# Kernel tuning notes

Measured on AMD Instinct MI355X. Metric: run time of the kernel, lower is better.

## Reference

```python
import jax, jax.numpy as jnp
import numpy as np

B, C, T, N = 8, 64, 24, 512
H = 2
D = C // H  # 32
NEG = -1e9
LN_EPS = 1e-5


def setup_inputs() -> dict:
    key = jax.random.key(0)
    ks = jax.random.split(key, 8)
    s = 1.0 / np.sqrt(C)
    return {
        "x": jax.random.normal(ks[0], (B, C, T, N), jnp.float32),
        "gso": jax.random.randint(ks[1], (N, N), 0, 2, jnp.int32),
        "Wq": jax.random.normal(ks[2], (C, C), jnp.float32) * s,
        "Wk": jax.random.normal(ks[3], (C, C), jnp.float32) * s,
        "Wv": jax.random.normal(ks[4], (C, C), jnp.float32) * s,
        "a_src": jax.random.normal(ks[5], (H, D), jnp.float32) * s,
        "a_dst": jax.random.normal(ks[6], (H, D), jnp.float32) * s,
        "gamma": jnp.ones((C,), jnp.float32),
        "beta": jnp.zeros((C,), jnp.float32),
    }


def reference(x, gso, Wq, Wk, Wv, a_src, a_dst, gamma, beta):
    # x: (B, C, T, N) -> (M, N, C) with M = B*T
    xr = jnp.transpose(x, (0, 2, 3, 1)).reshape(B * T, N, C)
    # torch Linear: y = x @ W.T ; split heads -> (M, N, H, D)
    Q = jnp.einsum('mnc,dc->mnd', xr, Wq).reshape(B * T, N, H, D)
    K = jnp.einsum('mnc,dc->mnd', xr, Wk).reshape(B * T, N, H, D)
    V = jnp.einsum('mnc,dc->mnd', xr, Wv).reshape(B * T, N, H, D)
    # additive GAT scores: s_ij = leaky_relu(<q_i, a_src> + <k_j, a_dst>)
    s_src = jnp.einsum('mnhd,hd->mhn', Q, a_src)  # (M, H, N)
    s_dst = jnp.einsum('mnhd,hd->mhn', K, a_dst)  # (M, H, N)
    scores = s_src[:, :, :, None] + s_dst[:, :, None, :]  # (M, H, N, N)
    scores = jax.nn.leaky_relu(scores, negative_slope=0.2)
    mask = jnp.where(gso == 0, jnp.float32(NEG), jnp.float32(0.0))  # (N, N)
    scores = scores + mask[None, None, :, :]
    attn = jax.nn.softmax(scores, axis=-1)  # dropout is identity in eval
    out = jnp.einsum('mhij,mjhd->mihd', attn, V).reshape(B * T, N, C)
    # LayerNorm over channels
    mu = jnp.mean(out, axis=-1, keepdims=True)
    var = jnp.var(out, axis=-1, keepdims=True)
    out = (out - mu) * jax.lax.rsqrt(var + LN_EPS) * gamma + beta
    # (M, N, C) -> (B, C, T, N)
    return jnp.transpose(out.reshape(B, T, N, C), (0, 3, 1, 2))
```

## Files before the change

### kernel.cpp

```cpp
#include <hip/hip_runtime.h>
#include <hip/hip_bf16.h>


#define NB 8
#define NC 64
#define NT 24
#define NN 512
#define LOG2E 1.44269504088896f

typedef float f32x4 __attribute__((ext_vector_type(4)));
typedef short bf16x8 __attribute__((ext_vector_type(8)));
typedef int   i32x4 __attribute__((ext_vector_type(4)));
typedef unsigned int u32;
typedef u32 u32x2 __attribute__((ext_vector_type(2)));

#ifndef __has_builtin
#define __has_builtin(x) 0
#endif

__device__ __forceinline__ float fast_exp2(float x) {
#if __has_builtin(__builtin_amdgcn_exp2f)
    return __builtin_amdgcn_exp2f(x);
#else
    return exp2f(x);
#endif
}

__device__ __forceinline__ u32 pk_bf16(float lo, float hi) {
    __hip_bfloat162 h2 = __float22bfloat162_rn(float2{lo, hi});
    u32 r; __builtin_memcpy(&r, &h2, 4); return r;
}
__device__ __forceinline__ unsigned short f2bfh(float f) {
    __hip_bfloat16 h = __float2bfloat16(f);
    unsigned short r; __builtin_memcpy(&r, &h, 2); return r;
}
__device__ __forceinline__ float bf2f(unsigned short s) {
    union { unsigned int u; float f; } v;
    v.u = ((unsigned int)s) << 16;
    return v.f;
}

#define VT2_IDX(k2,h,qq,dt,dl,e) \
    ((((((k2)*2+(h))*4+(qq))*2+(dt))*16+(dl))*8+(e))

#define XRB64(n,c) (((n)<<6) + (((((c)>>3) ^ ((n)&7))<<3) | ((c)&7)))

__global__ __launch_bounds__(512, 6)
void gat_one(const float* __restrict__ x, const int* __restrict__ gso,
             const float* __restrict__ Wq, const float* __restrict__ Wk,
             const float* __restrict__ Wv, const float* __restrict__ a_src,
             const float* __restrict__ a_dst, const float* __restrict__ gamma,
             const float* __restrict__ beta, float* __restrict__ out)
{
    __shared__ unsigned short sm_x[4096];
    __shared__ unsigned short sm_v[16384];
    __shared__ unsigned short sm_wvb[4096];
    __shared__ float sm_sdst[2][256];
    __shared__ float sm_ssrc[2][128];
    __shared__ float sm_wqa[2][NC];
    __shared__ float sm_wka[2][NC];

    const int bid  = blockIdx.x;
    const int m    = (bid >> 5) * 8 + (bid & 7);
    const int ch   = (bid >> 3) & 3;
    const int b    = m / NT;
    const int tt   = m % NT;
    const int tid  = threadIdx.x;
    const int lane = tid & 63;
    const int wid  = tid >> 6;
    const int fr   = lane & 15;
    const int fq   = lane >> 4;

    if (tid < 128) {
        const int h = tid >> 6, c = tid & 63;
        float aq = 0.f, ak = 0.f;
        #pragma unroll
        for (int d = 0; d < 32; ++d) {
            aq += Wq[(h*32 + d)*NC + c] * a_src[h*32 + d];
            ak += Wk[(h*32 + d)*NC + c] * a_dst[h*32 + d];
        }
        sm_wqa[h][c] = aq * LOG2E;
        sm_wka[h][c] = ak * LOG2E;
    }
    for (int idx = tid; idx < 4096; idx += 512) {
        const int e   = idx & 7;
        const int dl  = (idx >> 3) & 15;
        const int dt4 = (idx >> 7) & 3;
        const int qq  = (idx >> 9) & 3;
        const int ks  = idx >> 11;
        sm_wvb[idx] = f2bfh(Wv[(dt4*16 + dl)*NC + ks*32 + qq*8 + e]);
    }

    bf16x8 bones;
    {
        union { i32x4 i; bf16x8 h; } cv;
        const int w = (fr == 0) ? 0x3F803F80 : 0;
        cv.i[0] = w; cv.i[1] = w; cv.i[2] = w; cv.i[3] = w;
        bones = cv.h;
    }

    const int own_half = ch >> 1;
    const int ig = ch*128 + wid*16 + fr;
    float src0 = 0.f, src1 = 0.f;

    f32x4 acc[4] = {};
    f32x4 accs0 = {}, accs1 = {};

    #pragma unroll
    for (int pass = 0; pass < 2; ++pass) {
        const int hf = pass ? (1 - own_half) : own_half;

        for (int cidx = 0; cidx < 4; ++cidx) {
            const int nh0 = cidx * 64;
            const int ng0 = hf*256 + nh0;

            __syncthreads();

            {
                const int cb = wid * 8;
                float v[8];
                #pragma unroll
                for (int e = 0; e < 8; ++e)
                    v[e] = x[((size_t)(b*NC + cb + e)*NT + tt)*NN + ng0 + lane];
                i32x4 w;
                #pragma unroll
                for (int j = 0; j < 4; ++j)
                    w[j] = (int)pk_bf16(v[2*j], v[2*j+1]);
                *reinterpret_cast<i32x4*>(&sm_x[XRB64(lane, cb)]) = w;
            }
            __syncthreads();

            {
                const int nloc = tid >> 3;
                const int cp   = tid & 7;
                float sk0=0.f, sk1=0.f, sq0=0.f, sq1=0.f;
                #pragma unroll
                for (int i = 0; i < 8; ++i) {
                    const int c = cp*8 + i;
                    const float xv = bf2f(sm_x[XRB64(nloc, c)]);
                    sk0 += xv * sm_wka[0][c];
                    sk1 += xv * sm_wka[1][c];
                    sq0 += xv * sm_wqa[0][c];
                    sq1 += xv * sm_wqa[1][c];
                }
                sk0 += __shfl_xor(sk0,1); sk0 += __shfl_xor(sk0,2); sk0 += __shfl_xor(sk0,4);
                sk1 += __shfl_xor(sk1,1); sk1 += __shfl_xor(sk1,2); sk1 += __shfl_xor(sk1,4);
                sq0 += __shfl_xor(sq0,1); sq0 += __shfl_xor(sq0,2); sq0 += __shfl_xor(sq0,4);
                sq1 += __shfl_xor(sq1,1); sq1 += __shfl_xor(sq1,2); sq1 += __shfl_xor(sq1,4);
                if (cp == 0) {
                    sm_sdst[0][nh0 + nloc] = sk0;
                    sm_sdst[1][nh0 + nloc] = sk1;
                    if (pass == 0 && (cidx >> 1) == (ch & 1)) {
                        sm_ssrc[0][(cidx & 1)*64 + nloc] = sq0;
                        sm_ssrc[1][(cidx & 1)*64 + nloc] = sq1;
                    }
                }
            }

            {
                const int t = wid >> 1;
                const int h = wid & 1;
                f32x4 vacc[2] = {};
                #pragma unroll
                for (int ks = 0; ks < 2; ++ks) {
                    const bf16x8 af = *reinterpret_cast<const bf16x8*>(
                        &sm_x[XRB64(t*16 + fr, ks*32 + fq*8)]);
                    #pragma unroll
                    for (int dt = 0; dt < 2; ++dt) {
                        const int dt4 = h*2 + dt;
                        const bf16x8 bfv = *reinterpret_cast<const bf16x8*>(
                            &sm_wvb[(((ks*4 + fq)*4 + dt4)*16 + fr)*8]);
                        vacc[dt] = __builtin_amdgcn_mfma_f32_16x16x32_bf16(
                            af, bfv, vacc[dt], 0, 0, 0);
                    }
                }
                const int nh = nh0 + t*16 + 4*fq;
                #pragma unroll
                for (int dt = 0; dt < 2; ++dt) {
                    u32x2 dd;
                    dd[0] = pk_bf16(vacc[dt][0], vacc[dt][1]);
                    dd[1] = pk_bf16(vacc[dt][2], vacc[dt][3]);
                    *reinterpret_cast<u32x2*>(
                        &sm_v[VT2_IDX(nh>>5, h, (nh>>3)&3, dt, fr, nh&7)]) = dd;
                }
            }
        }
        __syncthreads();

        if (pass == 0) {
            src0 = sm_ssrc[0][wid*16 + fr];
            src1 = sm_ssrc[1][wid*16 + fr];
        }

        const int* gbase = &gso[(size_t)ig*NN + hf*256 + fq*8];
        for (int k2 = 0; k2 < 8; ++k2) {
            const int j0l = k2*32 + fq*8;
            const i32x4 g0 = *reinterpret_cast<const i32x4*>(gbase + k2*32);
            const i32x4 g1 = *reinterpret_cast<const i32x4*>(gbase + k2*32 + 4);
            const f32x4 da0 = *reinterpret_cast<const f32x4*>(&sm_sdst[0][j0l]);
            const f32x4 db0 = *reinterpret_cast<const f32x4*>(&sm_sdst[0][j0l+4]);
            const f32x4 da1 = *reinterpret_cast<const f32x4*>(&sm_sdst[1][j0l]);
            const f32x4 db1 = *reinterpret_cast<const f32x4*>(&sm_sdst[1][j0l+4]);

            u32 u0[8], u1[8];
            #pragma unroll
            for (int e = 0; e < 4; ++e) {
                float s0 = src0 + da0[e]; s0 = fmaxf(s0, 0.2f*s0);
                float s1 = src1 + da1[e]; s1 = fmaxf(s1, 0.2f*s1);
                const bool gb = (g0[e] != 0);
                u0[e] = gb ? __float_as_uint(fast_exp2(s0)) : 0u;
                u1[e] = gb ? __float_as_uint(fast_exp2(s1)) : 0u;
            }
            #pragma unroll
            for (int e = 0; e < 4; ++e) {
                float s0 = src0 + db0[e]; s0 = fmaxf(s0, 0.2f*s0);
                float s1 = src1 + db1[e]; s1 = fmaxf(s1, 0.2f*s1);
                const bool gb = (g1[e] != 0);
                u0[4+e] = gb ? __float_as_uint(fast_exp2(s0)) : 0u;
                u1[4+e] = gb ? __float_as_uint(fast_exp2(s1)) : 0u;
            }
            union { i32x4 i; bf16x8 h; } c0, c1;
            c0.i[0] = __builtin_amdgcn_perm(u0[1], u0[0], 0x07060302u);
            c0.i[1] = __builtin_amdgcn_perm(u0[3], u0[2], 0x07060302u);
            c0.i[2] = __builtin_amdgcn_perm(u0[5], u0[4], 0x07060302u);
            c0.i[3] = __builtin_amdgcn_perm(u0[7], u0[6], 0x07060302u);
            c1.i[0] = __builtin_amdgcn_perm(u1[1], u1[0], 0x07060302u);
            c1.i[1] = __builtin_amdgcn_perm(u1[3], u1[2], 0x07060302u);
            c1.i[2] = __builtin_amdgcn_perm(u1[5], u1[4], 0x07060302u);
            c1.i[3] = __builtin_amdgcn_perm(u1[7], u1[6], 0x07060302u);
            const bf16x8 af0 = c0.h, af1 = c1.h;

            accs0 = __builtin_amdgcn_mfma_f32_16x16x32_bf16(af0, bones, accs0, 0,0,0);
            {
                const bf16x8 b0 = *reinterpret_cast<const bf16x8*>(
                    &sm_v[VT2_IDX(k2,0,fq,0,fr,0)]);
                const bf16x8 b1 = *reinterpret_cast<const bf16x8*>(
                    &sm_v[VT2_IDX(k2,0,fq,1,fr,0)]);
                acc[0] = __builtin_amdgcn_mfma_f32_16x16x32_bf16(af0, b0, acc[0], 0,0,0);
                acc[1] = __builtin_amdgcn_mfma_f32_16x16x32_bf16(af0, b1, acc[1], 0,0,0);
            }
            accs1 = __builtin_amdgcn_mfma_f32_16x16x32_bf16(af1, bones, accs1, 0,0,0);
            {
                const bf16x8 b0 = *reinterpret_cast<const bf16x8*>(
                    &sm_v[VT2_IDX(k2,1,fq,0,fr,0)]);
                const bf16x8 b1 = *reinterpret_cast<const bf16x8*>(
                    &sm_v[VT2_IDX(k2,1,fq,1,fr,0)]);
                acc[2] = __builtin_amdgcn_mfma_f32_16x16x32_bf16(af1, b0, acc[2], 0,0,0);
                acc[3] = __builtin_amdgcn_mfma_f32_16x16x32_bf16(af1, b1, acc[3], 0,0,0);
            }
        }
    }

    float gmv[4], btv[4];
    #pragma unroll
    for (int dt4 = 0; dt4 < 4; ++dt4) {
        gmv[dt4] = gamma[dt4*16 + fr];
        btv[dt4] = beta [dt4*16 + fr];
    }
    #pragma unroll
    for (int rg = 0; rg < 4; ++rg) {
        const int rowloc = 4*fq + rg;
        const float rs0 = __shfl(accs0[rg], lane & 48);
        const float rs1 = __shfl(accs1[rg], lane & 48);
        const float inv0 = 1.f / rs0, inv1 = 1.f / rs1;
        float vv[4];
        vv[0] = acc[0][rg] * inv0;
        vv[1] = acc[1][rg] * inv0;
        vv[2] = acc[2][rg] * inv1;
        vv[3] = acc[3][rg] * inv1;
        float sum = vv[0]+vv[1]+vv[2]+vv[3];
        float ssq = vv[0]*vv[0]+vv[1]*vv[1]+vv[2]*vv[2]+vv[3]*vv[3];
        sum += __shfl_xor(sum,1); sum += __shfl_xor(sum,2);
        sum += __shfl_xor(sum,4); sum += __shfl_xor(sum,8);
        ssq += __shfl_xor(ssq,1); ssq += __shfl_xor(ssq,2);
        ssq += __shfl_xor(ssq,4); ssq += __shfl_xor(ssq,8);
        const float mu   = sum * (1.f/64.f);
        const float var  = ssq * (1.f/64.f) - mu*mu;
        const float rstd = rsqrtf(var + 1e-5f);
        const int irow = ch*128 + wid*16 + rowloc;
        #pragma unroll
        for (int dt4 = 0; dt4 < 4; ++dt4) {
            const float o = (vv[dt4] - mu) * rstd * gmv[dt4] + btv[dt4];
            out[((size_t)(b*NC + dt4*16 + fr)*NT + tt)*NN + irow] = o;
        }
    }
}

extern "C" void kernel_launch(void* const* d_in, const int* in_sizes, int n_in,
                              void* d_out, int out_size, void* d_ws, size_t ws_size,
                              hipStream_t stream) {
    (void)in_sizes; (void)n_in; (void)out_size; (void)d_ws; (void)ws_size;
    const float* x     = (const float*)d_in[0];
    const int*   gso   = (const int*)  d_in[1];
    const float* Wq    = (const float*)d_in[2];
    const float* Wk    = (const float*)d_in[3];
    const float* Wv    = (const float*)d_in[4];
    const float* a_src = (const float*)d_in[5];
    const float* a_dst = (const float*)d_in[6];
    const float* gamma = (const float*)d_in[7];
    const float* beta  = (const float*)d_in[8];
    float* out = (float*)d_out;

    gat_one<<<768, 512, 0, stream>>>(x, gso, Wq, Wk, Wv, a_src, a_dst,
                                     gamma, beta, out);
}
```

Measured before the change: 55.47 us.

## Factor leaky-relu exp into per-node exponentials and pipeline x loads over quarter chunks

The per-edge exp2 of leaky_relu(src+dst) is rewritten as max(E_i*F_j, E'_i*F'_j), where per-node exponentials for slope 1 and slope 0.2 are precomputed once per node. This removes transcendental work from the inner N×N loop. The loop now runs over four quarters of 128 nodes instead of two halves, which halves sm_v and allows 8 waves per SIMD in the launch bounds. The next chunk of x is register-prefetched so global loads overlap the compute. The risks are overflow or underflow in the factored exponentials, since there is no max subtraction, and more register pressure under the tighter occupancy bound.

```diff
diff --git a/kernel.cpp b/kernel.cpp
--- a/kernel.cpp
+++ b/kernel.cpp
@@ -45,7 +45,7 @@
 
 #define XRB64(n,c) (((n)<<6) + (((((c)>>3) ^ ((n)&7))<<3) | ((c)&7)))
 
-__global__ __launch_bounds__(512, 6)
+__global__ __launch_bounds__(512, 8)
 void gat_one(const float* __restrict__ x, const int* __restrict__ gso,
              const float* __restrict__ Wq, const float* __restrict__ Wk,
              const float* __restrict__ Wv, const float* __restrict__ a_src,
@@ -53,10 +53,10 @@
              const float* __restrict__ beta, float* __restrict__ out)
 {
     __shared__ unsigned short sm_x[4096];
-    __shared__ unsigned short sm_v[16384];
+    __shared__ unsigned short sm_v[8192];
     __shared__ unsigned short sm_wvb[4096];
-    __shared__ float sm_sdst[2][256];
-    __shared__ float sm_ssrc[2][128];
+    __shared__ float sm_sdst[2][2][128];
+    __shared__ float sm_ssrc[2][2][128];
     __shared__ float sm_wqa[2][NC];
     __shared__ float sm_wka[2][NC];
 
@@ -99,34 +99,43 @@
         bones = cv.h;
     }
 
-    const int own_half = ch >> 1;
     const int ig = ch*128 + wid*16 + fr;
-    float src0 = 0.f, src1 = 0.f;
-
+    const size_t xrow = ((size_t)(b*NC + wid*8)*NT + tt)*NN;
+
+    float vx[8];
+    {
+        const int ng0 = ch*128;
+        #pragma unroll
+        for (int e = 0; e < 8; ++e)
+            vx[e] = x[xrow + (size_t)e*NT*NN + ng0 + lane];
+    }
+
+    float Ei0 = 0.f, Ei0p = 0.f, Ei1 = 0.f, Ei1p = 0.f;
     f32x4 acc[4] = {};
     f32x4 accs0 = {}, accs1 = {};
 
-    #pragma unroll
-    for (int pass = 0; pass < 2; ++pass) {
-        const int hf = pass ? (1 - own_half) : own_half;
-
-        for (int cidx = 0; cidx < 4; ++cidx) {
-            const int nh0 = cidx * 64;
-            const int ng0 = hf*256 + nh0;
-
+    for (int t = 0; t < 4; ++t) {
+        const int q = (ch + t) & 3;
+
+        for (int c = 0; c < 2; ++c) {
             __syncthreads();
 
             {
-                const int cb = wid * 8;
-                float v[8];
-                #pragma unroll
-                for (int e = 0; e < 8; ++e)
-                    v[e] = x[((size_t)(b*NC + cb + e)*NT + tt)*NN + ng0 + lane];
                 i32x4 w;
                 #pragma unroll
                 for (int j = 0; j < 4; ++j)
-                    w[j] = (int)pk_bf16(v[2*j], v[2*j+1]);
-                *reinterpret_cast<i32x4*>(&sm_x[XRB64(lane, cb)]) = w;
+                    w[j] = (int)pk_bf16(vx[2*j], vx[2*j+1]);
+                *reinterpret_cast<i32x4*>(&sm_x[XRB64(lane, wid*8)]) = w;
+            }
+            {
+                const int s = t*2 + c;
+                if (s < 7) {
+                    const int qn  = (ch + ((s+1) >> 1)) & 3;
+                    const int ng0 = qn*128 + ((s+1) & 1)*64;
+                    #pragma unroll
+                    for (int e = 0; e < 8; ++e)
+                        vx[e] = x[xrow + (size_t)e*NT*NN + ng0 + lane];
+                }
             }
             __syncthreads();
 
@@ -136,35 +145,40 @@
                 float sk0=0.f, sk1=0.f, sq0=0.f, sq1=0.f;
                 #pragma unroll
                 for (int i = 0; i < 8; ++i) {
-                    const int c = cp*8 + i;
-                    const float xv = bf2f(sm_x[XRB64(nloc, c)]);
-                    sk0 += xv * sm_wka[0][c];
-                    sk1 += xv * sm_wka[1][c];
-                    sq0 += xv * sm_wqa[0][c];
-                    sq1 += xv * sm_wqa[1][c];
+                    const int cc = cp*8 + i;
+                    const float xv = bf2f(sm_x[XRB64(nloc, cc)]);
+                    sk0 += xv * sm_wka[0][cc];
+                    sk1 += xv * sm_wka[1][cc];
+                    sq0 += xv * sm_wqa[0][cc];
+                    sq1 += xv * sm_wqa[1][cc];
                 }
                 sk0 += __shfl_xor(sk0,1); sk0 += __shfl_xor(sk0,2); sk0 += __shfl_xor(sk0,4);
                 sk1 += __shfl_xor(sk1,1); sk1 += __shfl_xor(sk1,2); sk1 += __shfl_xor(sk1,4);
                 sq0 += __shfl_xor(sq0,1); sq0 += __shfl_xor(sq0,2); sq0 += __shfl_xor(sq0,4);
                 sq1 += __shfl_xor(sq1,1); sq1 += __shfl_xor(sq1,2); sq1 += __shfl_xor(sq1,4);
                 if (cp == 0) {
-                    sm_sdst[0][nh0 + nloc] = sk0;
-                    sm_sdst[1][nh0 + nloc] = sk1;
-                    if (pass == 0 && (cidx >> 1) == (ch & 1)) {
-                        sm_ssrc[0][(cidx & 1)*64 + nloc] = sq0;
-                        sm_ssrc[1][(cidx & 1)*64 + nloc] = sq1;
+                    const int jl = c*64 + nloc;
+                    sm_sdst[0][0][jl] = fast_exp2(sk0);
+                    sm_sdst[0][1][jl] = fast_exp2(0.2f*sk0);
+                    sm_sdst[1][0][jl] = fast_exp2(sk1);
+                    sm_sdst[1][1][jl] = fast_exp2(0.2f*sk1);
+                    if (t == 0) {
+                        sm_ssrc[0][0][jl] = fast_exp2(sq0);
+                        sm_ssrc[0][1][jl] = fast_exp2(0.2f*sq0);
+                        sm_ssrc[1][0][jl] = fast_exp2(sq1);
+                        sm_ssrc[1][1][jl] = fast_exp2(0.2f*sq1);
                     }
                 }
             }
 
             {
-                const int t = wid >> 1;
-                const int h = wid & 1;
+                const int nt4 = wid >> 1;
+                const int h   = wid & 1;
                 f32x4 vacc[2] = {};
                 #pragma unroll
                 for (int ks = 0; ks < 2; ++ks) {
                     const bf16x8 af = *reinterpret_cast<const bf16x8*>(
-                        &sm_x[XRB64(t*16 + fr, ks*32 + fq*8)]);
+                        &sm_x[XRB64(nt4*16 + fr, ks*32 + fq*8)]);
                     #pragma unroll
                     for (int dt = 0; dt < 2; ++dt) {
                         const int dt4 = h*2 + dt;
@@ -174,7 +188,7 @@
                             af, bfv, vacc[dt], 0, 0, 0);
                     }
                 }
-                const int nh = nh0 + t*16 + 4*fq;
+                const int nh = c*64 + nt4*16 + 4*fq;
                 #pragma unroll
                 for (int dt = 0; dt < 2; ++dt) {
                     u32x2 dd;
@@ -187,37 +201,43 @@
         }
         __syncthreads();
 
-        if (pass == 0) {
-            src0 = sm_ssrc[0][wid*16 + fr];
-            src1 = sm_ssrc[1][wid*16 + fr];
-        }
-
-        const int* gbase = &gso[(size_t)ig*NN + hf*256 + fq*8];
-        for (int k2 = 0; k2 < 8; ++k2) {
+        if (t == 0) {
+            Ei0  = sm_ssrc[0][0][wid*16 + fr];
+            Ei0p = sm_ssrc[0][1][wid*16 + fr];
+            Ei1  = sm_ssrc[1][0][wid*16 + fr];
+            Ei1p = sm_ssrc[1][1][wid*16 + fr];
+        }
+
+        const int* gbase = &gso[(size_t)ig*NN + q*128 + fq*8];
+        for (int k2 = 0; k2 < 4; ++k2) {
             const int j0l = k2*32 + fq*8;
             const i32x4 g0 = *reinterpret_cast<const i32x4*>(gbase + k2*32);
             const i32x4 g1 = *reinterpret_cast<const i32x4*>(gbase + k2*32 + 4);
-            const f32x4 da0 = *reinterpret_cast<const f32x4*>(&sm_sdst[0][j0l]);
-            const f32x4 db0 = *reinterpret_cast<const f32x4*>(&sm_sdst[0][j0l+4]);
-            const f32x4 da1 = *reinterpret_cast<const f32x4*>(&sm_sdst[1][j0l]);
-            const f32x4 db1 = *reinterpret_cast<const f32x4*>(&sm_sdst[1][j0l+4]);
+            const f32x4 Fa0  = *reinterpret_cast<const f32x4*>(&sm_sdst[0][0][j0l]);
+            const f32x4 Fb0  = *reinterpret_cast<const f32x4*>(&sm_sdst[0][0][j0l+4]);
+            const f32x4 Fpa0 = *reinterpret_cast<const f32x4*>(&sm_sdst[0][1][j0l]);
+            const f32x4 Fpb0 = *reinterpret_cast<const f32x4*>(&sm_sdst[0][1][j0l+4]);
+            const f32x4 Fa1  = *reinterpret_cast<const f32x4*>(&sm_sdst[1][0][j0l]);
+            const f32x4 Fb1  = *reinterpret_cast<const f32x4*>(&sm_sdst[1][0][j0l+4]);
+            const f32x4 Fpa1 = *reinterpret_cast<const f32x4*>(&sm_sdst[1][1][j0l]);
+            const f32x4 Fpb1 = *reinterpret_cast<const f32x4*>(&sm_sdst[1][1][j0l+4]);
 
             u32 u0[8], u1[8];
             #pragma unroll
             for (int e = 0; e < 4; ++e) {
-                float s0 = src0 + da0[e]; s0 = fmaxf(s0, 0.2f*s0);
-                float s1 = src1 + da1[e]; s1 = fmaxf(s1, 0.2f*s1);
+                const float w0 = fmaxf(Ei0*Fa0[e], Ei0p*Fpa0[e]);
+                const float w1 = fmaxf(Ei1*Fa1[e], Ei1p*Fpa1[e]);
                 const bool gb = (g0[e] != 0);
-                u0[e] = gb ? __float_as_uint(fast_exp2(s0)) : 0u;
-                u1[e] = gb ? __float_as_uint(fast_exp2(s1)) : 0u;
+                u0[e] = gb ? __float_as_uint(w0) : 0u;
+                u1[e] = gb ? __float_as_uint(w1) : 0u;
             }
             #pragma unroll
             for (int e = 0; e < 4; ++e) {
-                float s0 = src0 + db0[e]; s0 = fmaxf(s0, 0.2f*s0);
-                float s1 = src1 + db1[e]; s1 = fmaxf(s1, 0.2f*s1);
+                const float w0 = fmaxf(Ei0*Fb0[e], Ei0p*Fpb0[e]);
+                const float w1 = fmaxf(Ei1*Fb1[e], Ei1p*Fpb1[e]);
                 const bool gb = (g1[e] != 0);
-                u0[4+e] = gb ? __float_as_uint(fast_exp2(s0)) : 0u;
-                u1[4+e] = gb ? __float_as_uint(fast_exp2(s1)) : 0u;
+                u0[4+e] = gb ? __float_as_uint(w0) : 0u;
+                u1[4+e] = gb ? __float_as_uint(w1) : 0u;
             }
             union { i32x4 i; bf16x8 h; } c0, c1;
             c0.i[0] = __builtin_amdgcn_perm(u0[1], u0[0], 0x07060302u);
```

New measurement: 80.40 us, median of 2. 44.9% more time.
